# Kernel tuning notes

Hardware: AMD Instinct MI355X
Metric: run time of the kernel (lower is better)

## Reference

```python
import jax, jax.numpy as jnp
import numpy as np

EPS = 1e-5
N_NODES = 50000


def gcn_conv(x, edge_index, W, b):
    # PyG GCNConv: add self-loops, symmetric deg normalization, then aggregate.
    n = x.shape[0]
    loop = jnp.arange(n)
    src = jnp.concatenate([edge_index[0], loop])
    dst = jnp.concatenate([edge_index[1], loop])
    deg = jax.ops.segment_sum(jnp.ones_like(dst, dtype=x.dtype), dst, num_segments=n)
    dinv = jnp.where(deg > 0, jax.lax.rsqrt(deg), 0.0)
    norm = dinv[src] * dinv[dst]                     # [E+N]
    xw = x @ W                                        # [N, out]
    msg = xw[src] * norm[:, None]                     # gather + scale
    out = jax.ops.segment_sum(msg, dst, num_segments=n)
    return out + b


def batch_norm(x, gamma, beta):
    # training-mode BatchNorm1d: batch statistics, biased variance
    m = x.mean(0)
    v = ((x - m) ** 2).mean(0)
    return (x - m) * jax.lax.rsqrt(v + EPS) * gamma + beta


def rnn(x, Wih, Whh, bih, bhh):
    # torch nn.RNN (tanh), 1 layer, batch=1, seq over nodes; h0 = zeros
    h0 = jnp.zeros((Whh.shape[0],), dtype=x.dtype)
    def step(h, xt):
        h = jnp.tanh(xt @ Wih.T + bih + h @ Whh.T + bhh)
        return h, h
    _, ys = jax.lax.scan(step, h0, x)
    return ys  # [N, 50]


def setup_inputs() -> dict:
    key = jax.random.key(0)
    ks = jax.random.split(key, 30)
    def rn(k, shape, scale):
        return jax.random.normal(k, shape, dtype=jnp.float32) * scale
    inp = {}
    inp['x'] = rn(ks[0], (N_NODES, 100), 1.0)
    inp['edge_index'] = jax.random.randint(ks[1], (2, 800000), 0, N_NODES, dtype=jnp.int64)
    # GCNConv weights [in, out] + bias
    inp['W1'] = rn(ks[2], (100, 100), 0.1); inp['b1'] = rn(ks[3], (100,), 0.1)
    inp['W2'] = rn(ks[4], (100, 100), 0.1); inp['b2'] = rn(ks[5], (100,), 0.1)
    # batch norms (affine)
    inp['g1'] = jnp.ones((100,), jnp.float32); inp['be1'] = jnp.zeros((100,), jnp.float32)
    inp['g2'] = jnp.ones((100,), jnp.float32); inp['be2'] = jnp.zeros((100,), jnp.float32)
    inp['g3'] = jnp.ones((50,), jnp.float32);  inp['be3'] = jnp.zeros((50,), jnp.float32)
    inp['g4'] = jnp.ones((30,), jnp.float32);  inp['be4'] = jnp.zeros((30,), jnp.float32)
    # RNN params (torch layout: [hidden, in], [hidden, hidden])
    inp['Wih'] = rn(ks[6], (50, 100), 0.1); inp['Whh'] = rn(ks[7], (50, 50), 0.1)
    inp['bih'] = rn(ks[8], (50,), 0.1);     inp['bhh'] = rn(ks[9], (50,), 0.1)
    # Linears (torch layout [out, in])
    inp['lw1'] = rn(ks[10], (50, 50), 0.1); inp['lb1'] = rn(ks[11], (50,), 0.1)
    inp['lw2'] = rn(ks[12], (30, 50), 0.1); inp['lb2'] = rn(ks[13], (30,), 0.1)
    inp['lw3'] = rn(ks[14], (30, 30), 0.1); inp['lb3'] = rn(ks[15], (30,), 0.1)
    return inp


def reference(x, edge_index, W1, b1, W2, b2, g1, be1, g2, be2, g3, be3, g4, be4,
              Wih, Whh, bih, bhh, lw1, lb1, lw2, lb2, lw3, lb3):
    h = gcn_conv(x, edge_index, W1, b1)
    h = jax.nn.relu(batch_norm(h, g1, be1))
    h = gcn_conv(h, edge_index, W2, b2)
    h = batch_norm(h, g2, be2)
    h = rnn(h, Wih, Whh, bih, bhh)            # [N, 50]
    h = h @ lw1.T + lb1
    h = jax.nn.relu(batch_norm(h, g3, be3))
    h = h @ lw2.T + lb2
    h = jax.nn.relu(batch_norm(h, g4, be4))
    h = h @ lw3.T + lb3
    return jax.nn.log_softmax(h, axis=1)      # [N, 30]
```

## Files before the change

kernel.cpp:

```cpp
#include <hip/hip_runtime.h>
#include <hip/hip_fp16.h>
#include <math.h>

#define NN 50000
#define NE 800000
#define CAP 96

typedef _Float16 h8 __attribute__((ext_vector_type(8)));
typedef float    fv4 __attribute__((ext_vector_type(4)));

static inline int cdiv(long a, int b){ return (int)((a + (long)b - 1) / b); }

__global__ void k_scatter(const int* __restrict__ ei, int* __restrict__ cur,
                          int* __restrict__ ssrc, int E){
  int i = blockIdx.x*blockDim.x + threadIdx.x;
  if (i >= E) return;
  int s = ei[i];
  int d = ei[E + i];
  int p = atomicAdd(&cur[d], 1);
  if (p < CAP) ssrc[(long)d*CAP + p] = s;
}

__global__ void k_dinv(const int* __restrict__ cnt, float* __restrict__ dinv, int n){
  int i = blockIdx.x*blockDim.x + threadIdx.x;
  if (i < n) dinv[i] = rsqrtf((float)cnt[i] + 1.0f);
}

__global__ void k_trh(const float* __restrict__ W1, const float* __restrict__ W2,
                      const float* __restrict__ wih, const float* __restrict__ l1,
                      const float* __restrict__ l2,  const float* __restrict__ l3,
                      _Float16* __restrict__ w1t, _Float16* __restrict__ w2t,
                      _Float16* __restrict__ wihh, _Float16* __restrict__ l1h,
                      _Float16* __restrict__ l2h, float* __restrict__ l3f)
{
  int i = blockIdx.x*blockDim.x + threadIdx.x;
  if (i < 14336) { int n=i>>7, k=i&127; w1t[i] = (_Float16)((n<100&&k<100)? W1[k*100+n] : 0.f); return; }
  i -= 14336;
  if (i < 14336) { int n=i>>7, k=i&127; w2t[i] = (_Float16)((n<100&&k<100)? W2[k*100+n] : 0.f); return; }
  i -= 14336;
  if (i < 8192)  { int n=i>>7, k=i&127; wihh[i] = (_Float16)((n<50&&k<100)? wih[n*100+k] : 0.f); return; }
  i -= 8192;
  if (i < 4096)  { int n=i>>6, k=i&63;  l1h[i] = (_Float16)((n<50&&k<50)? l1[n*50+k] : 0.f); return; }
  i -= 4096;
  if (i < 2048)  { int n=i>>6, k=i&63;  l2h[i] = (_Float16)((n<30&&k<50)? l2[n*50+k] : 0.f); return; }
  i -= 2048;
  if (i < 960)   { int k=i>>5, c=i&31;  l3f[i] = (c<30)? l3[c*30+k] : 0.f; return; }
}

__global__ void k_gather(const __half* __restrict__ xws, const int* __restrict__ ssrc,
                         const int* __restrict__ cnt, const float* __restrict__ dinv,
                         const float* __restrict__ bias, float* __restrict__ out)
{
  int d = blockIdx.x;
  int c = threadIdx.x;
  if (c >= 100) return;
  int n = min(cnt[d], CAP);
  const int* sl = ssrc + (long)d*CAP;
  float a0 = __half2float(xws[(long)d*100 + c]);
  float a1 = 0.f, a2 = 0.f, a3 = 0.f;
  int i = 0;
  for (; i + 4 <= n; i += 4) {
    int s0 = sl[i], s1 = sl[i+1], s2 = sl[i+2], s3 = sl[i+3];
    a0 += __half2float(xws[(long)s0*100 + c]);
    a1 += __half2float(xws[(long)s1*100 + c]);
    a2 += __half2float(xws[(long)s2*100 + c]);
    a3 += __half2float(xws[(long)s3*100 + c]);
  }
  for (; i < n; ++i) a0 += __half2float(xws[(long)sl[i]*100 + c]);
  float acc = (a0 + a1) + (a2 + a3);
  out[(long)d*100 + c] = fmaf(dinv[d], acc, bias[c]);
}

template<int KO,int KS,int NT,int CO,int BNIN,int RELUIN,int NB,int OUTH>
__global__ void __launch_bounds__(256) k_mfma(
    const float* __restrict__ A, const _Float16* __restrict__ Wt,
    const float* __restrict__ bias1, const float* __restrict__ bias2,
    const float* __restrict__ sc, const float* __restrict__ sh,
    const float* __restrict__ dinv, void* __restrict__ outv, int rows)
{
  constexpr int KP  = KS*32;
  constexpr int LDA = KP + 8;
  __shared__ _Float16 Ah[64 * LDA];
  const int tid = threadIdx.x;
  const int r0  = blockIdx.x * 64;

  for (int e = tid; e < 64*(KO/2); e += 256) {
    int rr = e / (KO/2);
    int kk = (e - rr*(KO/2)) * 2;
    int gr = r0 + rr;
    float v0 = 0.f, v1 = 0.f;
    if (gr < rows) {
      float2 t = *(const float2*)(A + (long)gr*KO + kk);
      v0 = t.x; v1 = t.y;
      if (BNIN) {
        v0 = fmaf(v0, sc[kk],   sh[kk]);   if (RELUIN) v0 = fmaxf(v0, 0.f);
        v1 = fmaf(v1, sc[kk+1], sh[kk+1]); if (RELUIN) v1 = fmaxf(v1, 0.f);
      }
    }
    Ah[rr*LDA + kk]     = (_Float16)v0;
    Ah[rr*LDA + kk + 1] = (_Float16)v1;
  }
  if (KP > KO) {
    for (int e = tid; e < 64*(KP-KO); e += 256) {
      int rr = e / (KP-KO), kk = KO + (e - rr*(KP-KO));
      Ah[rr*LDA + kk] = (_Float16)0.f;
    }
  }
  __syncthreads();

  const int wave = tid >> 6, lane = tid & 63;
  const int m = lane & 15, q = lane >> 4;
  const int row = wave*16 + m;
  h8 af[KS];
  #pragma unroll
  for (int ks = 0; ks < KS; ++ks)
    af[ks] = *(const h8*)(Ah + row*LDA + ks*32 + q*8);

  const int grb = r0 + wave*16 + q*4;
  #pragma unroll
  for (int nt = 0; nt < NT; ++nt) {
    fv4 acc = {0.f, 0.f, 0.f, 0.f};
    #pragma unroll
    for (int ks = 0; ks < KS; ++ks) {
      h8 bf = *(const h8*)(Wt + (long)(nt*16 + m)*KP + ks*32 + q*8);
      acc = __builtin_amdgcn_mfma_f32_16x16x32_f16(af[ks], bf, acc, 0, 0, 0);
    }
    int c = nt*16 + m;
    if (c < CO) {
      float bi = 0.f;
      if (NB >= 1) bi = bias1[c];
      if (NB == 2) bi += bias2[c];
      #pragma unroll
      for (int i = 0; i < 4; ++i) {
        int gr = grb + i;
        if (gr < rows) {
          if (OUTH) ((__half*)outv)[(long)gr*CO + c] = __float2half(acc[i] * dinv[gr]);
          else      ((float*)outv)[(long)gr*CO + c] = acc[i] + bi;
        }
      }
    }
  }
}

template<int K, int C, int WC, int CT>
__global__ void __launch_bounds__(64) k_tgemm_lsm(
    const float* __restrict__ A, const float* __restrict__ W,
    const float* __restrict__ bias1,
    const float* __restrict__ sc, const float* __restrict__ sh,
    float* __restrict__ out, int rows)
{
  constexpr int TM  = 64;
  constexpr int LDK = K + 1;
  __shared__ __align__(16) float As[TM * LDK];
  __shared__ __align__(16) float Ws[K * WC + 16];
  const int tid = threadIdx.x;
  const int r0  = blockIdx.x * TM;

  for (int e = tid; e < K*WC/4; e += TM) {
    float4 t = *(const float4*)(W + 4*e);
    *(float4*)(Ws + 4*e) = t;
  }
  for (int e = tid; e < TM*K/2; e += TM) {
    int idx = e * 2;
    int rr  = idx / K;
    int kk  = idx - rr*K;
    int gr  = r0 + rr;
    float v0 = 0.f, v1 = 0.f;
    if (gr < rows) {
      float2 t = *(const float2*)(A + (long)gr*K + kk);
      v0 = fmaxf(fmaf(t.x, sc[kk],   sh[kk]),   0.f);
      v1 = fmaxf(fmaf(t.y, sc[kk+1], sh[kk+1]), 0.f);
    }
    As[rr*LDK + kk] = v0;
    As[rr*LDK + kk + 1] = v1;
  }
  __syncthreads();

  const int r = tid;
  float acc[CT];
  #pragma unroll
  for (int j = 0; j < CT; ++j) acc[j] = (j < C) ? bias1[j] : 0.f;
  #pragma unroll 2
  for (int k = 0; k < K; ++k) {
    float a = As[r*LDK + k];
    const float* p = Ws + k*WC;
    #pragma unroll
    for (int qd = 0; qd < CT/4; ++qd) {
      float4 t = *(const float4*)(p + 4*qd);
      acc[4*qd+0] = fmaf(a, t.x, acc[4*qd+0]);
      acc[4*qd+1] = fmaf(a, t.y, acc[4*qd+1]);
      acc[4*qd+2] = fmaf(a, t.z, acc[4*qd+2]);
      acc[4*qd+3] = fmaf(a, t.w, acc[4*qd+3]);
    }
  }
  int gr = r0 + r;
  if (gr >= rows) return;
  float mx = acc[0];
  #pragma unroll
  for (int j = 1; j < C; ++j) mx = fmaxf(mx, acc[j]);
  float s = 0.0f;
  #pragma unroll
  for (int j = 0; j < C; ++j) s += expf(acc[j] - mx);
  float l = mx + logf(s);
  float* o = out + (long)gr*C;
  #pragma unroll
  for (int j = 0; j < C; ++j) o[j] = acc[j] - l;
}

__global__ void k_bn_stats(const float* __restrict__ x, float* __restrict__ sums,
                           float* __restrict__ sqs, int rows, int C)
{
  int c = threadIdx.x;
  if (c >= C) return;
  float s = 0.0f, q = 0.0f;
  for (int r = blockIdx.x; r < rows; r += gridDim.x) {
    float v = x[(long)r*C + c];
    s += v;
    q = fmaf(v, v, q);
  }
  atomicAdd(&sums[c], s);
  atomicAdd(&sqs[c], q);
}

__global__ void k_bn_fin(const float* __restrict__ sums, const float* __restrict__ sqs,
                         const float* __restrict__ g, const float* __restrict__ be,
                         float* __restrict__ sc, float* __restrict__ sh, int C, float invN)
{
  int c = threadIdx.x;
  if (c >= C) return;
  float m = sums[c]*invN;
  float v = fmaxf(sqs[c]*invN - m*m, 0.0f);
  float s = g[c]*rsqrtf(v + 1e-5f);
  sc[c] = s;
  sh[c] = be[c] - m*s;
}

__device__ __forceinline__ float fast_tanh(float z){
  float az = fabsf(z);
  float e  = __expf(2.0f*az);
  float t  = 1.0f - 2.0f*__builtin_amdgcn_rcpf(e + 1.0f);
  return copysignf(t, z);
}

__device__ __forceinline__ float rlane(float v, int l){
  return __uint_as_float(__builtin_amdgcn_readlane(__float_as_uint(v), l));
}

__global__ void __launch_bounds__(64,1) k_rnn_par(const float* __restrict__ u,
                                                  const float* __restrict__ Whh,
                                                  float* __restrict__ ys,
                                                  int N, int L, int W)
{
  const int lane = threadIdx.x;
  const int li = min(lane, 49);
  const int t0 = blockIdx.x * L;
  if (t0 >= N) return;
  const int t1 = min(t0 + L, N);
  const int ts = max(0, t0 - W);

  float one;
  asm volatile("v_mov_b32 %0, 1.0" : "=v"(one));
  float w[50];
  #pragma unroll
  for (int j = 0; j < 50; ++j) w[j] = Whh[li*50 + j] * one;

  const float* up = u + (long)ts*50 + li;
  float r0 = up[0];
  float r1 = up[50];
  up += 100;

  float h = 0.0f;

#define RNN_STEP(STORE)                                         \
  {                                                             \
    float ucur = r0; r0 = r1; r1 = up[0]; up += 50;             \
    float a0 = 0.f, a1 = 0.f, a2 = 0.f, a3 = 0.f;               \
    _Pragma("unroll")                                           \
    for (int j = 0; j < 48; j += 4) {                           \
      a0 = fmaf(w[j+0], rlane(h, j+0), a0);                     \
      a1 = fmaf(w[j+1], rlane(h, j+1), a1);                     \
      a2 = fmaf(w[j+2], rlane(h, j+2), a2);                     \
      a3 = fmaf(w[j+3], rlane(h, j+3), a3);                     \
    }                                                           \
    a0 = fmaf(w[48], rlane(h, 48), a0);                         \
    a1 = fmaf(w[49], rlane(h, 49), a1);                         \
    h = fast_tanh(ucur + (a0 + a1) + (a2 + a3));                \
    if (STORE && lane < 50) ys[(long)t*50 + lane] = h;          \
  }

  for (int t = ts; t < t0; ++t) RNN_STEP(0)
  for (int t = t0; t < t1; ++t) RNN_STEP(1)
#undef RNN_STEP
}

extern "C" void kernel_launch(void* const* d_in, const int* in_sizes, int n_in,
                              void* d_out, int out_size, void* d_ws, size_t ws_size,
                              hipStream_t stream)
{
  const float* x   = (const float*)d_in[0];
  const int*   ei  = (const int*)  d_in[1];
  const float* W1  = (const float*)d_in[2];
  const float* b1  = (const float*)d_in[3];
  const float* W2  = (const float*)d_in[4];
  const float* b2  = (const float*)d_in[5];
  const float* g1  = (const float*)d_in[6];
  const float* be1 = (const float*)d_in[7];
  const float* g2  = (const float*)d_in[8];
  const float* be2 = (const float*)d_in[9];
  const float* g3  = (const float*)d_in[10];
  const float* be3 = (const float*)d_in[11];
  const float* g4  = (const float*)d_in[12];
  const float* be4 = (const float*)d_in[13];
  const float* Wih = (const float*)d_in[14];
  const float* Whh = (const float*)d_in[15];
  const float* bih = (const float*)d_in[16];
  const float* bhh = (const float*)d_in[17];
  const float* lw1 = (const float*)d_in[18];
  const float* lb1 = (const float*)d_in[19];
  const float* lw2 = (const float*)d_in[20];
  const float* lb2 = (const float*)d_in[21];
  const float* lw3 = (const float*)d_in[22];
  const float* lb3 = (const float*)d_in[23];
  float* out = (float*)d_out;

  float* bufA = (float*)d_ws;
  float* bufB = bufA + 5000000;
  float* bufC = bufB + 5000000;
  float* st   = bufC + 5000000;
  int*   cur  = (int*)(st + 8*128);
  float* scsh = (float*)(cur + NN);
  float* dinv = scsh + 8*128;
  int*   ssrc = (int*)(dinv + NN);
  _Float16* wh = (_Float16*)(ssrc + (long)NN*CAP);
  _Float16* w1t  = wh;
  _Float16* w2t  = wh + 14336;
  _Float16* wihh = wh + 28672;
  _Float16* l1h  = wh + 36864;
  _Float16* l2h  = wh + 40960;
  float*    l3f  = (float*)(wh + 43008);

  __half* xwh = (__half*)bufA;

  float* sums1 = st + 0*128; float* sqs1 = st + 1*128;
  float* sums2 = st + 2*128; float* sqs2 = st + 3*128;
  float* sums3 = st + 4*128; float* sqs3 = st + 5*128;
  float* sums4 = st + 6*128; float* sqs4 = st + 7*128;
  float* sc1 = scsh + 0*128; float* sh1 = scsh + 1*128;
  float* sc2 = scsh + 2*128; float* sh2 = scsh + 3*128;
  float* sc3 = scsh + 4*128; float* sh3 = scsh + 5*128;
  float* sc4 = scsh + 6*128; float* sh4 = scsh + 7*128;

  const int B = 256;
  const float invN = 1.0f / (float)NN;
  const int statsGrid = 784;
  const int gt = cdiv(NN, 64);

  hipMemsetAsync(st, 0, 8*128*sizeof(float) + NN*sizeof(int), stream);

  k_trh<<<cdiv(43968,B), B, 0, stream>>>(W1, W2, Wih, lw1, lw2, lw3,
                                         w1t, w2t, wihh, l1h, l2h, l3f);
  k_scatter<<<cdiv(NE,B), B, 0, stream>>>(ei, cur, ssrc, NE);
  k_dinv   <<<cdiv(NN,B), B, 0, stream>>>(cur, dinv, NN);

  k_mfma<100,4,7,100,0,0,0,1><<<gt, 256, 0, stream>>>(x, w1t, nullptr, nullptr, nullptr, nullptr, dinv, xwh, NN);
  k_gather<<<NN, 128, 0, stream>>>(xwh, ssrc, cur, dinv, b1, bufB);
  k_bn_stats<<<statsGrid, 128, 0, stream>>>(bufB, sums1, sqs1, NN, 100);
  k_bn_fin<<<1, 128, 0, stream>>>(sums1, sqs1, g1, be1, sc1, sh1, 100, invN);

  k_mfma<100,4,7,100,1,1,0,1><<<gt, 256, 0, stream>>>(bufB, w2t, nullptr, nullptr, sc1, sh1, dinv, xwh, NN);
  k_gather<<<NN, 128, 0, stream>>>(xwh, ssrc, cur, dinv, b2, bufC);
  k_bn_stats<<<statsGrid, 128, 0, stream>>>(bufC, sums2, sqs2, NN, 100);
  k_bn_fin<<<1, 128, 0, stream>>>(sums2, sqs2, g2, be2, sc2, sh2, 100, invN);

  k_mfma<100,4,4,50,1,0,2,0><<<gt, 256, 0, stream>>>(bufC, wihh, bih, bhh, sc2, sh2, nullptr, bufA, NN);
  {
    const int L = 32, W = 48;
    k_rnn_par<<<cdiv(NN,L), 64, 0, stream>>>(bufA, Whh, bufB, NN, L, W);
  }

  k_mfma<50,2,4,50,0,0,1,0><<<gt, 256, 0, stream>>>(bufB, l1h, lb1, nullptr, nullptr, nullptr, nullptr, bufC, NN);
  k_bn_stats<<<statsGrid, 64, 0, stream>>>(bufC, sums3, sqs3, NN, 50);
  k_bn_fin<<<1, 64, 0, stream>>>(sums3, sqs3, g3, be3, sc3, sh3, 50, invN);

  k_mfma<50,2,2,30,1,1,1,0><<<gt, 256, 0, stream>>>(bufC, l2h, lb2, nullptr, sc3, sh3, nullptr, bufA, NN);
  k_bn_stats<<<statsGrid, 64, 0, stream>>>(bufA, sums4, sqs4, NN, 30);
  k_bn_fin<<<1, 64, 0, stream>>>(sums4, sqs4, g4, be4, sc4, sh4, 30, invN);

  k_tgemm_lsm<30,30,32,32><<<gt, 64, 0, stream>>>(bufA, l3f, lb3, sc4, sh4, out, NN);
}
```

Baseline: 520.7 us.

## Build CSR adjacency with 16-bit indices and fold BN finalize into consumers

Replaces the fixed-capacity per-node bucket array with a CSR layout built by count, single-block prefix scan, and scatter, storing source indices as 16-bit values. This shrinks the index footprint and removes the capacity truncation, at the cost of an extra counting pass and a serial-ish one-block scan. BatchNorm scale/shift finalization is moved into the consuming GEMM kernels' prologue, removing four tiny launches but recomputing per block.

```diff
diff --git a/kernel.cpp b/kernel.cpp
--- a/kernel.cpp
+++ b/kernel.cpp
@@ -4,26 +4,55 @@
 
 #define NN 50000
 #define NE 800000
-#define CAP 96
 
 typedef _Float16 h8 __attribute__((ext_vector_type(8)));
 typedef float    fv4 __attribute__((ext_vector_type(4)));
 
 static inline int cdiv(long a, int b){ return (int)((a + (long)b - 1) / b); }
 
+__global__ void k_count(const int* __restrict__ dst, int* __restrict__ cnt, int E){
+  int i = blockIdx.x*blockDim.x + threadIdx.x;
+  if (i < E) atomicAdd(&cnt[dst[i]], 1);
+}
+
+__global__ void __launch_bounds__(1024) k_scan(const int* __restrict__ cnt,
+                                               int* __restrict__ off, int* __restrict__ cur,
+                                               float* __restrict__ dinv, int n)
+{
+  __shared__ int ps[1024];
+  const int tid = threadIdx.x;
+  const int chunk = (n + 1023) / 1024;
+  int b = tid * chunk;
+  int e = min(b + chunk, n);
+  int s = 0;
+  for (int i = b; i < e; ++i) s += cnt[i];
+  ps[tid] = s;
+  __syncthreads();
+  for (int d = 1; d < 1024; d <<= 1) {
+    int v = (tid >= d) ? ps[tid - d] : 0;
+    __syncthreads();
+    ps[tid] += v;
+    __syncthreads();
+  }
+  int run = (tid > 0) ? ps[tid - 1] : 0;
+  for (int i = b; i < e; ++i) {
+    int c = cnt[i];
+    off[i] = run;
+    cur[i] = run;
+    dinv[i] = rsqrtf((float)c + 1.0f);
+    run += c;
+  }
+  if (tid == 1023) off[n] = ps[1023];
+}
+
 __global__ void k_scatter(const int* __restrict__ ei, int* __restrict__ cur,
-                          int* __restrict__ ssrc, int E){
+                          unsigned short* __restrict__ ssrc, int E){
   int i = blockIdx.x*blockDim.x + threadIdx.x;
   if (i >= E) return;
   int s = ei[i];
   int d = ei[E + i];
   int p = atomicAdd(&cur[d], 1);
-  if (p < CAP) ssrc[(long)d*CAP + p] = s;
-}
-
-__global__ void k_dinv(const int* __restrict__ cnt, float* __restrict__ dinv, int n){
-  int i = blockIdx.x*blockDim.x + threadIdx.x;
-  if (i < n) dinv[i] = rsqrtf((float)cnt[i] + 1.0f);
+  ssrc[p] = (unsigned short)s;
 }
 
 __global__ void k_trh(const float* __restrict__ W1, const float* __restrict__ W2,
@@ -47,26 +76,25 @@
   if (i < 960)   { int k=i>>5, c=i&31;  l3f[i] = (c<30)? l3[c*30+k] : 0.f; return; }
 }
 
-__global__ void k_gather(const __half* __restrict__ xws, const int* __restrict__ ssrc,
-                         const int* __restrict__ cnt, const float* __restrict__ dinv,
+__global__ void k_gather(const __half* __restrict__ xws, const unsigned short* __restrict__ ssrc,
+                         const int* __restrict__ off, const float* __restrict__ dinv,
                          const float* __restrict__ bias, float* __restrict__ out)
 {
   int d = blockIdx.x;
   int c = threadIdx.x;
   if (c >= 100) return;
-  int n = min(cnt[d], CAP);
-  const int* sl = ssrc + (long)d*CAP;
+  int b = off[d], e = off[d+1];
   float a0 = __half2float(xws[(long)d*100 + c]);
   float a1 = 0.f, a2 = 0.f, a3 = 0.f;
-  int i = 0;
-  for (; i + 4 <= n; i += 4) {
-    int s0 = sl[i], s1 = sl[i+1], s2 = sl[i+2], s3 = sl[i+3];
+  int i = b;
+  for (; i + 4 <= e; i += 4) {
+    int s0 = ssrc[i], s1 = ssrc[i+1], s2 = ssrc[i+2], s3 = ssrc[i+3];
     a0 += __half2float(xws[(long)s0*100 + c]);
     a1 += __half2float(xws[(long)s1*100 + c]);
     a2 += __half2float(xws[(long)s2*100 + c]);
     a3 += __half2float(xws[(long)s3*100 + c]);
   }
-  for (; i < n; ++i) a0 += __half2float(xws[(long)sl[i]*100 + c]);
+  for (; i < e; ++i) a0 += __half2float(xws[(long)ssrc[i]*100 + c]);
   float acc = (a0 + a1) + (a2 + a3);
   out[(long)d*100 + c] = fmaf(dinv[d], acc, bias[c]);
 }
@@ -75,14 +103,27 @@
 __global__ void __launch_bounds__(256) k_mfma(
     const float* __restrict__ A, const _Float16* __restrict__ Wt,
     const float* __restrict__ bias1, const float* __restrict__ bias2,
-    const float* __restrict__ sc, const float* __restrict__ sh,
-    const float* __restrict__ dinv, void* __restrict__ outv, int rows)
+    const float* __restrict__ sums, const float* __restrict__ sqs,
+    const float* __restrict__ gw, const float* __restrict__ be,
+    const float* __restrict__ dinv, void* __restrict__ outv, int rows, float invN)
 {
   constexpr int KP  = KS*32;
   constexpr int LDA = KP + 8;
   __shared__ _Float16 Ah[64 * LDA];
+  __shared__ float scS[BNIN ? KO : 1], shS[BNIN ? KO : 1];
   const int tid = threadIdx.x;
   const int r0  = blockIdx.x * 64;
+
+  if (BNIN) {
+    for (int c = tid; c < KO; c += 256) {
+      float m = sums[c]*invN;
+      float v = fmaxf(sqs[c]*invN - m*m, 0.f);
+      float s = gw[c]*rsqrtf(v + 1e-5f);
+      scS[c] = s;
+      shS[c] = be[c] - m*s;
+    }
+    __syncthreads();
+  }
 
   for (int e = tid; e < 64*(KO/2); e += 256) {
     int rr = e / (KO/2);
@@ -93,8 +134,8 @@
       float2 t = *(const float2*)(A + (long)gr*KO + kk);
       v0 = t.x; v1 = t.y;
       if (BNIN) {
-        v0 = fmaf(v0, sc[kk],   sh[kk]);   if (RELUIN) v0 = fmaxf(v0, 0.f);
-        v1 = fmaf(v1, sc[kk+1], sh[kk+1]); if (RELUIN) v1 = fmaxf(v1, 0.f);
+        v0 = fmaf(v0, scS[kk],   shS[kk]);   if (RELUIN) v0 = fmaxf(v0, 0.f);
+        v1 = fmaf(v1, scS[kk+1], shS[kk+1]); if (RELUIN) v1 = fmaxf(v1, 0.f);
       }
     }
     Ah[rr*LDA + kk]     = (_Float16)v0;
@@ -146,15 +187,26 @@
 __global__ void __launch_bounds__(64) k_tgemm_lsm(
     const float* __restrict__ A, const float* __restrict__ W,
     const float* __restrict__ bias1,
-    const float* __restrict__ sc, const float* __restrict__ sh,
-    float* __restrict__ out, int rows)
+    const float* __restrict__ sums, const float* __restrict__ sqs,
+    const float* __restrict__ gw, const float* __restrict__ be,
+    float* __restrict__ out, int rows, float invN)
 {
   constexpr int TM  = 64;
   constexpr int LDK = K + 1;
   __shared__ __align__(16) float As[TM * LDK];
   __shared__ __align__(16) float Ws[K * WC + 16];
+  __shared__ float scS[K], shS[K];
   const int tid = threadIdx.x;
   const int r0  = blockIdx.x * TM;
+
+  if (tid < K) {
+    float m = sums[tid]*invN;
+    float v = fmaxf(sqs[tid]*invN - m*m, 0.f);
+    float s = gw[tid]*rsqrtf(v + 1e-5f);
+    scS[tid] = s;
+    shS[tid] = be[tid] - m*s;
+  }
+  __syncthreads();
 
   for (int e = tid; e < K*WC/4; e += TM) {
     float4 t = *(const float4*)(W + 4*e);
@@ -168,8 +220,8 @@
     float v0 = 0.f, v1 = 0.f;
     if (gr < rows) {
       float2 t = *(const float2*)(A + (long)gr*K + kk);
-      v0 = fmaxf(fmaf(t.x, sc[kk],   sh[kk]),   0.f);
-      v1 = fmaxf(fmaf(t.y, sc[kk+1], sh[kk+1]), 0.f);
+      v0 = fmaxf(fmaf(t.x, scS[kk],   shS[kk]),   0.f);
+      v1 = fmaxf(fmaf(t.y, scS[kk+1], shS[kk+1]), 0.f);
     }
     As[rr*LDK + kk] = v0;
     As[rr*LDK + kk + 1] = v1;
@@ -220,19 +272,6 @@
   }
   atomicAdd(&sums[c], s);
   atomicAdd(&sqs[c], q);
-}
-
-__global__ void k_bn_fin(const float* __restrict__ sums, const float* __restrict__ sqs,
-                         const float* __restrict__ g, const float* __restrict__ be,
-                         float* __restrict__ sc, float* __restrict__ sh, int C, float invN)
-{
-  int c = threadIdx.x;
-  if (c >= C) return;
-  float m = sums[c]*invN;
-  float v = fmaxf(sqs[c]*invN - m*m, 0.0f);
-  float s = g[c]*rsqrtf(v + 1e-5f);
-  sc[c] = s;
-  sh[c] = be[c] - m*s;
 }
 
 __device__ __forceinline__ float fast_tanh(float z){
@@ -327,11 +366,12 @@
   float* bufB = bufA + 5000000;
   float* bufC = bufB + 5000000;
   float* st   = bufC + 5000000;
-  int*   cur  = (int*)(st + 8*128);
-  float* scsh = (float*)(cur + NN);
-  float* dinv = scsh + 8*128;
-  int*   ssrc = (int*)(dinv + NN);
-  _Float16* wh = (_Float16*)(ssrc + (long)NN*CAP);
+  int*   cnt  = (int*)(st + 8*128);
+  int*   cur  = cnt + NN;
+  int*   off  = cur + NN;
+  float* dinv = (float*)(off + NN + 1);
+  unsigned short* ssrc = (unsigned short*)(dinv + NN);
+  _Float16* wh = (_Float16*)(ssrc + NE);
   _Float16* w1t  = wh;
   _Float16* w2t  = wh + 14336;
   _Float16* wihh = wh + 28672;
@@ -345,10 +385,6 @@
   float* sums2 = st + 2*128; float* sqs2 = st + 3*128;
   float* sums3 = st + 4*128; float* sqs3 = st + 5*128;
   float* sums4 = st + 6*128; float* sqs4 = st + 7*128;
-  float* sc1 = scsh + 0*128; float* sh1 = scsh + 1*128;
-  float* sc2 = scsh + 2*128; float* sh2 = scsh + 3*128;
-  float* sc3 = scsh + 4*128; float* sh3 = scsh + 5*128;
-  float* sc4 = scsh + 6*128; float* sh4 = scsh + 7*128;
 
   const int B = 256;
   const float invN = 1.0f / (float)NN;
@@ -359,32 +395,35 @@
 
   k_trh<<<cdiv(43968,B), B, 0, stream>>>(W1, W2, Wih, lw1, lw2, lw3,
                                          w1t, w2t, wihh, l1h, l2h, l3f);
+  k_count<<<cdiv(NE,B), B, 0, stream>>>(ei + NE, cnt, NE);
+  k_scan<<<1, 1024, 0, stream>>>(cnt, off, cur, dinv, NN);
   k_scatter<<<cdiv(NE,B), B, 0, stream>>>(ei, cur, ssrc, NE);
-  k_dinv   <<<cdiv(NN,B), B, 0, stream>>>(cur, dinv, NN);
-
-  k_mfma<100,4,7,100,0,0,0,1><<<gt, 256, 0, stream>>>(x, w1t, nullptr, nullptr, nullptr, nullptr, dinv, xwh, NN);
-  k_gather<<<NN, 128, 0, stream>>>(xwh, ssrc, cur, dinv, b1, bufB);
+
+  k_mfma<100,4,7,100,0,0,0,1><<<gt, 256, 0, stream>>>(x, w1t, nullptr, nullptr,
+      nullptr, nullptr, nullptr, nullptr, dinv, xwh, NN, invN);
+  k_gather<<<NN, 128, 0, stream>>>(xwh, ssrc, off, dinv, b1, bufB);
   k_bn_stats<<<statsGrid, 128, 0, stream>>>(bufB, sums1, sqs1, NN, 100);
-  k_bn_fin<<<1, 128, 0, stream>>>(sums1, sqs1, g1, be1, sc1, sh1, 100, invN);
-
-  k_mfma<100,4,7,100,1,1,0,1><<<gt, 256, 0, stream>>>(bufB, w2t, nullptr, nullptr, sc1, sh1, dinv, xwh, NN);
-  k_gather<<<NN, 128, 0, stream>>>(xwh, ssrc, cur, dinv, b2, bufC);
+
+  k_mfma<100,4,7,100,1,1,0,1><<<gt, 256, 0, stream>>>(bufB, w2t, nullptr, nullptr,
+      sums1, sqs1, g1, be1, dinv, xwh, NN, invN);
+  k_gather<<<NN, 128, 0, stream>>>(xwh, ssrc, off, dinv, b2, bufC);
   k_bn_stats<<<statsGrid, 128, 0, stream>>>(bufC, sums2, sqs2, NN, 100);
-  k_bn_fin<<<1, 128, 0, stream>>>(sums2, sqs2, g2, be2, sc2, sh2, 100, invN);
-
-  k_mfma<100,4,4,50,1,0,2,0><<<gt, 256, 0, stream>>>(bufC, wihh, bih, bhh, sc2, sh2, nullptr, bufA, NN);
+
+  k_mfma<100,4,4,50,1,0,2,0><<<gt, 256, 0, stream>>>(bufC, wihh, bih, bhh,
+      sums2, sqs2, g2, be2, nullptr, bufA, NN, invN);
   {
     const int L = 32, W = 48;
     k_rnn_par<<<cdiv(NN,L), 64, 0, stream>>>(bufA, Whh, bufB, NN, L, W);
   }
 
-  k_mfma<50,2,4,50,0,0,1,0><<<gt, 256, 0, stream>>>(bufB, l1h, lb1, nullptr, nullptr, nullptr, nullptr, bufC, NN);
+  k_mfma<50,2,4,50,0,0,1,0><<<gt, 256, 0, stream>>>(bufB, l1h, lb1, nullptr,
+      nullptr, nullptr, nullptr, nullptr, nullptr, bufC, NN, invN);
   k_bn_stats<<<statsGrid, 64, 0, stream>>>(bufC, sums3, sqs3, NN, 50);
-  k_bn_fin<<<1, 64, 0, stream>>>(sums3, sqs3, g3, be3, sc3, sh3, 50, invN);
-
-  k_mfma<50,2,2,30,1,1,1,0><<<gt, 256, 0, stream>>>(bufC, l2h, lb2, nullptr, sc3, sh3, nullptr, bufA, NN);
+
+  k_mfma<50,2,2,30,1,1,1,0><<<gt, 256, 0, stream>>>(bufC, l2h, lb2, nullptr,
+      sums3, sqs3, g3, be3, nullptr, bufA, NN, invN);
   k_bn_stats<<<statsGrid, 64, 0, stream>>>(bufA, sums4, sqs4, NN, 30);
-  k_bn_fin<<<1, 64, 0, stream>>>(sums4, sqs4, g4, be4, sc4, sh4, 30, invN);
-
-  k_tgemm_lsm<30,30,32,32><<<gt, 64, 0, stream>>>(bufA, l3f, lb3, sc4, sh4, out, NN);
-}
+
+  k_tgemm_lsm<30,30,32,32><<<gt, 64, 0, stream>>>(bufA, l3f, lb3,
+      sums4, sqs4, g4, be4, out, NN, invN);
+}
```

New measurement: 698.7 us. 1.34x slower.
